# Kernel optimization log

Measured on AMD Instinct MI355X. Metric: run time of the kernel, lower is better.

## Reference

```python
import jax, jax.numpy as jnp
import numpy as np

L, H, A, E, V = 2, 512, 200, 512, 10000
SOS_ID = 0


def setup_inputs() -> dict:
    key = jax.random.key(0)
    ks = jax.random.split(key, 20)
    B, T, S = 64, 512, 128
    s = 0.02
    d = {}
    d["encoder_outputs"] = jax.random.normal(ks[0], (L, T, B, H), jnp.float32)
    d["encoder_final_states"] = jax.random.normal(ks[1], (L, B, H), jnp.float32)
    d["targets"] = jax.random.randint(ks[2], (B, S), 0, V)
    # Bahdanau attention params (per RNN layer)
    d["Qw"] = jax.random.normal(ks[3], (L, A, H), jnp.float32) * s
    d["Qb"] = jnp.zeros((L, A), jnp.float32)
    d["Kw"] = jax.random.normal(ks[4], (L, A, H), jnp.float32) * s
    d["Kb"] = jnp.zeros((L, A), jnp.float32)
    d["Vw"] = jax.random.normal(ks[5], (L, A), jnp.float32) * s
    d["Vb"] = jnp.zeros((L,), jnp.float32)
    # embedding table
    d["emb_table"] = jax.random.normal(ks[6], (V, E), jnp.float32) * s
    # 2-layer GRU (torch layout: W_ih (3H, in), W_hh (3H, H))
    d["Wih0"] = jax.random.normal(ks[7], (3 * H, E + H), jnp.float32) * s
    d["Whh0"] = jax.random.normal(ks[8], (3 * H, H), jnp.float32) * s
    d["bih0"] = jnp.zeros((3 * H,), jnp.float32)
    d["bhh0"] = jnp.zeros((3 * H,), jnp.float32)
    d["Wih1"] = jax.random.normal(ks[9], (3 * H, H), jnp.float32) * s
    d["Whh1"] = jax.random.normal(ks[10], (3 * H, H), jnp.float32) * s
    d["bih1"] = jnp.zeros((3 * H,), jnp.float32)
    d["bhh1"] = jnp.zeros((3 * H,), jnp.float32)
    # output projection (single Linear: decoder_projection=[])
    d["Pw"] = jax.random.normal(ks[11], (V, H), jnp.float32) * s
    d["Pb"] = jnp.zeros((V,), jnp.float32)
    return d


def _gru_cell(x, h, Wih, Whh, bih, bhh):
    gi = x @ Wih.T + bih
    gh = h @ Whh.T + bhh
    ir, iz, inn = jnp.split(gi, 3, axis=-1)
    hr, hz, hn = jnp.split(gh, 3, axis=-1)
    r = jax.nn.sigmoid(ir + hr)
    z = jax.nn.sigmoid(iz + hz)
    n = jnp.tanh(inn + r * hn)
    return (1.0 - z) * n + z * h


def reference(encoder_outputs, encoder_final_states, targets, Qw, Qb, Kw, Kb, Vw, Vb,
              emb_table, Wih0, Whh0, bih0, bhh0, Wih1, Whh1, bih1, bhh1, Pw, Pb):
    B, S = targets.shape
    # teacher forcing: input at step i is SOS for i=0 else targets[:, i-1]
    tok = jnp.concatenate([jnp.full((B, 1), SOS_ID, targets.dtype), targets[:, :-1]], axis=1)
    # keys don't change across steps -> precompute key projection: (L, T, B, A)
    k_proj = jnp.einsum('lah,ltbh->ltba', Kw, encoder_outputs) + Kb[:, None, None, :]

    def step(h, tok_t):
        # Bahdanau attention (softmax jointly over layers and time, per batch col)
        q = jnp.einsum('lah,lbh->lba', Qw, h) + Qb[:, None, :]          # (L,B,A)
        e = jnp.tanh(q[:, None] + k_proj)                                # (L,T,B,A)
        scores = jnp.einsum('la,ltba->ltb', Vw, e) + Vb[:, None, None]   # (L,T,B)
        w = jax.nn.softmax(scores.reshape(L * scores.shape[1], B), axis=0).reshape(scores.shape)
        context = jnp.einsum('ltb,ltbh->bh', w, encoder_outputs)         # (B,H)
        # embedding (+relu; dropout=0 / eval), concat with context
        x = jnp.concatenate([jax.nn.relu(emb_table[tok_t]), context], axis=-1)  # (B, E+H)
        h0 = _gru_cell(x, h[0], Wih0, Whh0, bih0, bhh0)
        h1 = _gru_cell(h0, h[1], Wih1, Whh1, bih1, bhh1)
        logits = h1 @ Pw.T + Pb                                           # (B,V)
        return jnp.stack([h0, h1]), logits

    _, logits = jax.lax.scan(step, encoder_final_states, tok.T)  # over S steps
    return jnp.transpose(logits, (1, 0, 2))  # (B, S, V)
```

## Files before the change

### kernel.cpp

```cpp
#include <hip/hip_runtime.h>


#define DEV __device__ __forceinline__

DEV float bf2f(unsigned short u) {
    unsigned int x = ((unsigned int)u) << 16;
    return __builtin_bit_cast(float, x);
}
DEV unsigned short f2bf(float f) {
    unsigned int x = __builtin_bit_cast(unsigned int, f);
    unsigned int r = (x + 0x7FFFu + ((x >> 16) & 1u)) >> 16;
    return (unsigned short)r;
}
DEV float fin(float v) {
    unsigned int b = __builtin_bit_cast(unsigned int, v);
    return ((b & 0x7F800000u) == 0x7F800000u) ? 1000.0f : v;
}
DEV float rcp_f(float x) { return __builtin_amdgcn_rcpf(x); }
DEV float sigm_f(float x) {
    x = fminf(fmaxf(x, -30.f), 30.f);
    float e = __expf(-x);
    return rcp_f(1.f + e);
}
DEV float tanh_f(float x) {
    x = fminf(fmaxf(x, -15.f), 15.f);
    float ex = __expf(2.f * x);
    return 1.f - 2.f * rcp_f(1.f + ex);
}

typedef __attribute__((ext_vector_type(8))) short short8;
typedef __attribute__((ext_vector_type(4))) float float4v;

__global__ __launch_bounds__(256) void detect_k(const unsigned short* __restrict__ raw,
                                                int* __restrict__ flag) {
    __shared__ int cnt;
    if (threadIdx.x == 0) cnt = 0;
    __syncthreads();
    long idx = 2L * ((long)threadIdx.x * 997 + 13);
    unsigned short u = raw[idx];
    unsigned int e = (u >> 7) & 0xFF;
    if (e >= 0x81) atomicAdd(&cnt, 1);
    __syncthreads();
    if (threadIdx.x == 0) *flag = (cnt >= 40) ? 1 : 0;
}

__global__ __launch_bounds__(256) void conv_k(const void* __restrict__ src,
                                              unsigned short* __restrict__ dst, long n,
                                              const int* __restrict__ flag) {
    int f = *flag;
    long i0 = (long)blockIdx.x * 256 + threadIdx.x;
    long st = (long)gridDim.x * 256;
    if (f) {
        const float* s = (const float*)src;
        for (long i = i0; i < n; i += st) dst[i] = f2bf(s[i]);
    } else {
        const unsigned short* s = (const unsigned short*)src;
        for (long i = i0; i < n; i += st) dst[i] = s[i];
    }
}

__global__ __launch_bounds__(256) void init_ht_k(const void* __restrict__ ef,
                                                 float* __restrict__ hT,
                                                 const int* __restrict__ flag) {
    int f = *flag;
    int i = blockIdx.x * 256 + threadIdx.x;
    int l = i >> 15, rem = i & 32767, b = rem >> 9, h = rem & 511;
    float v = f ? ((const float*)ef)[i] : bf2f(((const unsigned short*)ef)[i]);
    hT[(l * 512 + h) * 64 + b] = v;
}

__global__ __launch_bounds__(256) void mfma_gemm_k(
    const unsigned short* __restrict__ A, const void* __restrict__ BtV,
    const void* __restrict__ biasV, void* __restrict__ dstV, int Nlim, int mode,
    long Az, long Bz, long biasz, const int* __restrict__ flagp) {
    const int K = 512;
    int f = (mode == 1) ? *flagp : 0;
    int l = blockIdx.z;
    const unsigned short* Ab = A + (long)l * Az;
    const unsigned short* Bb = (const unsigned short*)BtV + (long)l * Bz;
    const float* Bf = (const float*)BtV + (long)l * Bz;
    int tid = threadIdx.x;
    int lane = tid & 63, wid = tid >> 6;
    int wy = wid >> 1, wx = wid & 1;
    int quad = lane >> 4, r16 = lane & 15;
    int m0 = blockIdx.x * 128 + wy * 64;
    int n0 = blockIdx.y * 128 + wx * 64;

    float4v acc[4][4];
    for (int i = 0; i < 4; ++i)
        for (int j = 0; j < 4; ++j) acc[i][j] = (float4v){0.f, 0.f, 0.f, 0.f};

    for (int kt = 0; kt < K / 32; ++kt) {
        int k0 = kt * 32 + quad * 8;
        short8 af[4], bfr[4];
#pragma unroll
        for (int mi = 0; mi < 4; ++mi) {
            int row = m0 + mi * 16 + r16;
            af[mi] = *(const short8*)(Ab + (long)row * K + k0);
        }
#pragma unroll
        for (int ni = 0; ni < 4; ++ni) {
            int col = n0 + ni * 16 + r16;
            if (col < Nlim) {
                if (f) {
                    short8 t;
#pragma unroll
                    for (int j = 0; j < 8; ++j)
                        t[j] = (short)f2bf(Bf[(long)col * K + k0 + j]);
                    bfr[ni] = t;
                } else {
                    bfr[ni] = *(const short8*)(Bb + (long)col * K + k0);
                }
            } else {
                bfr[ni] = (short8){0, 0, 0, 0, 0, 0, 0, 0};
            }
        }
#pragma unroll
        for (int mi = 0; mi < 4; ++mi)
#pragma unroll
            for (int ni = 0; ni < 4; ++ni)
                acc[mi][ni] = __builtin_amdgcn_mfma_f32_16x16x32_bf16(
                    af[mi], bfr[ni], acc[mi][ni], 0, 0, 0);
    }

    unsigned short* dstu = (unsigned short*)dstV;
    float* dstf = (float*)dstV;
    for (int mi = 0; mi < 4; ++mi)
        for (int ni = 0; ni < 4; ++ni) {
            int n = n0 + ni * 16 + r16;
            if (n >= Nlim) continue;
            float bv;
            if (mode == 0)
                bv = bf2f(((const unsigned short*)biasV)[l * biasz + n]);
            else
                bv = f ? ((const float*)biasV)[n] : bf2f(((const unsigned short*)biasV)[n]);
#pragma unroll
            for (int r = 0; r < 4; ++r) {
                int m = m0 + mi * 16 + quad * 4 + r;
                float v = fin(acc[mi][ni][r] + bv);
                if (mode == 0) {
                    int t = m >> 6, b = m & 63;
                    dstu[(((long)(l * 512 + t) * 200 + n) * 64 + b)] = f2bf(v);
                } else {
                    int s = m >> 6, b = m & 63;
                    long oi = ((long)b * 128 + s) * 10000 + n;
                    if (f) dstf[oi] = v;
                    else dstu[oi] = f2bf(v);
                }
            }
        }
}

__global__ __launch_bounds__(256) void q_k(const unsigned short* __restrict__ Qw,
                                           const unsigned short* __restrict__ Qb,
                                           const float* __restrict__ hT,
                                           float* __restrict__ q) {
    __shared__ float red[4][64];
    int blk = blockIdx.x;
    int l = blk / 200, a = blk % 200;
    int tid = threadIdx.x, w = tid >> 6, lane = tid & 63;
    const unsigned short* qr = Qw + (l * 200 + a) * 512;
    const float* hb = hT + l * 512 * 64;
    float acc = 0.f;
    int h0 = w * 128;
    for (int h = h0; h < h0 + 128; h += 8) {
        uint4 u = *(const uint4*)(qr + h);
        const unsigned short* us = (const unsigned short*)&u;
#pragma unroll
        for (int j = 0; j < 8; ++j) acc = fmaf(bf2f(us[j]), hb[(h + j) * 64 + lane], acc);
    }
    red[w][lane] = acc;
    __syncthreads();
    if (w == 0) {
        float v = red[0][lane] + red[1][lane] + red[2][lane] + red[3][lane] +
                  bf2f(Qb[l * 200 + a]);
        q[(l * 200 + a) * 64 + lane] = v;
    }
}

__global__ __launch_bounds__(256) void step1_k(
    const unsigned short* __restrict__ kp, const float* __restrict__ q,
    float* __restrict__ sc, const unsigned short* __restrict__ Vw,
    const unsigned short* __restrict__ Vb, const float* __restrict__ hT,
    const unsigned short* __restrict__ Whh0, const unsigned short* __restrict__ Whh1,
    const unsigned short* __restrict__ bhh0, const unsigned short* __restrict__ bhh1,
    float* __restrict__ gh, const unsigned short* __restrict__ emb,
    const int* __restrict__ tgt, float* __restrict__ xT, int s) {
    int blk = blockIdx.x, tid = threadIdx.x, w = tid >> 6, lane = tid & 63;
    if (blk < 256) {
        int l = blk >> 7, tc = blk & 127, t = tc * 4 + w;
        const unsigned short* kr = kp + (size_t)((l * 512 + t) * 200) * 64;
        const float* qb = q + (l * 200) * 64;
        float acc = 0.f;
#pragma unroll 4
        for (int a = 0; a < 200; ++a) {
            float x = bf2f(kr[a * 64 + lane]) + qb[a * 64 + lane];
            acc = fmaf(bf2f(Vw[l * 200 + a]), tanh_f(x), acc);
        }
        sc[(l * 512 + t) * 64 + lane] = acc + bf2f(Vb[l]);
    } else if (blk < 1024) {
        int widx = (blk - 256) * 4 + w;
        int layer = widx / 1536, j = widx % 1536;
        const unsigned short* Wr = (layer ? Whh1 : Whh0) + (size_t)j * 512;
        const float* hb = hT + layer * 512 * 64;
        float acc = 0.f;
        for (int h = 0; h < 512; h += 8) {
            uint4 u = *(const uint4*)(Wr + h);
            const unsigned short* us = (const unsigned short*)&u;
#pragma unroll
            for (int jj = 0; jj < 8; ++jj)
                acc = fmaf(bf2f(us[jj]), hb[(h + jj) * 64 + lane], acc);
        }
        acc += bf2f((layer ? bhh1 : bhh0)[j]);
        gh[(layer * 1536 + j) * 64 + lane] = acc;
    } else {
        int eb = blk - 1024;
        for (int it = 0; it < 16; ++it) {
            int i = eb * 4096 + it * 256 + tid;
            int b = i >> 9, k = i & 511;
            int tok = (s == 0) ? 0 : tgt[b * 128 + (s - 1)];
            tok = tok < 0 ? 0 : (tok > 9999 ? 9999 : tok);
            float v = bf2f(emb[(size_t)tok * 512 + k]);
            xT[k * 64 + b] = v > 0.f ? v : 0.f;
        }
    }
}

__global__ __launch_bounds__(256) void ctx_k(const float* __restrict__ sc,
                                             const unsigned short* __restrict__ enc,
                                             float* __restrict__ xT) {
    __shared__ float wbuf[1024];
    __shared__ float rbuf[256];
    int blk = blockIdx.x, tid = threadIdx.x;
    int b = blk >> 2, hq = blk & 3;

    float s0[4];
    float lm = -3.0e38f;
#pragma unroll
    for (int i = 0; i < 4; ++i) {
        float v = sc[(tid + i * 256) * 64 + b];
        v = fminf(fmaxf(v, -1.0e30f), 1.0e30f);
        s0[i] = v;
        lm = fmaxf(lm, v);
    }
    rbuf[tid] = lm;
    __syncthreads();
    for (int off = 128; off > 0; off >>= 1) {
        if (tid < off) rbuf[tid] = fmaxf(rbuf[tid], rbuf[tid + off]);
        __syncthreads();
    }
    float M = rbuf[0];
    __syncthreads();
    float ls = 0.f;
#pragma unroll
    for (int i = 0; i < 4; ++i) {
        float e = __expf(fmaxf(s0[i] - M, -80.f));
        wbuf[tid + i * 256] = e;
        ls += e;
    }
    rbuf[tid] = ls;
    __syncthreads();
    for (int off = 128; off > 0; off >>= 1) {
        if (tid < off) rbuf[tid] += rbuf[tid + off];
        __syncthreads();
    }
    float rinv = 1.0f / rbuf[0];

    int h = hq * 128 + (tid & 127), half = tid >> 7;
    float acc = 0.f;
#pragma unroll 8
    for (int lt = half * 512; lt < half * 512 + 512; ++lt)
        acc = fmaf(wbuf[lt], bf2f(enc[((size_t)lt * 64 + b) * 512 + h]), acc);
    __syncthreads();
    rbuf[tid] = acc;
    __syncthreads();
    if (tid < 128)
        xT[(512 + hq * 128 + tid) * 64 + b] = (rbuf[tid] + rbuf[tid + 128]) * rinv;
}

__global__ __launch_bounds__(256) void gru0_k(const float* __restrict__ xT,
                                              const unsigned short* __restrict__ Wih0,
                                              const unsigned short* __restrict__ bih0,
                                              const float* __restrict__ gh,
                                              float* __restrict__ hT) {
    __shared__ float red[4][6][64];
    int blk = blockIdx.x, tid = threadIdx.x, w = tid >> 6, lane = tid & 63;
    int jj0 = blk * 2;
    const unsigned short* r_[6];
    r_[0] = Wih0 + (size_t)(jj0) * 1024;
    r_[1] = Wih0 + (size_t)(jj0 + 1) * 1024;
    r_[2] = Wih0 + (size_t)(jj0 + 512) * 1024;
    r_[3] = Wih0 + (size_t)(jj0 + 513) * 1024;
    r_[4] = Wih0 + (size_t)(jj0 + 1024) * 1024;
    r_[5] = Wih0 + (size_t)(jj0 + 1025) * 1024;
    float acc[6] = {0.f, 0.f, 0.f, 0.f, 0.f, 0.f};
    int k0 = w * 256;
    for (int k = k0; k < k0 + 256; k += 8) {
        uint4 u[6];
#pragma unroll
        for (int i = 0; i < 6; ++i) u[i] = *(const uint4*)(r_[i] + k);
#pragma unroll
        for (int j = 0; j < 8; ++j) {
            float xv = xT[(k + j) * 64 + lane];
#pragma unroll
            for (int i = 0; i < 6; ++i)
                acc[i] = fmaf(bf2f(((const unsigned short*)&u[i])[j]), xv, acc[i]);
        }
    }
#pragma unroll
    for (int i = 0; i < 6; ++i) red[w][i][lane] = acc[i];
    __syncthreads();
    if (w == 0) {
#pragma unroll
        for (int d = 0; d < 2; ++d) {
            int j = jj0 + d;
            float gir = red[0][0 + d][lane] + red[1][0 + d][lane] + red[2][0 + d][lane] +
                        red[3][0 + d][lane] + bf2f(bih0[j]);
            float giz = red[0][2 + d][lane] + red[1][2 + d][lane] + red[2][2 + d][lane] +
                        red[3][2 + d][lane] + bf2f(bih0[512 + j]);
            float gin = red[0][4 + d][lane] + red[1][4 + d][lane] + red[2][4 + d][lane] +
                        red[3][4 + d][lane] + bf2f(bih0[1024 + j]);
            float r = sigm_f(gir + gh[j * 64 + lane]);
            float z = sigm_f(giz + gh[(512 + j) * 64 + lane]);
            float n = tanh_f(gin + r * gh[(1024 + j) * 64 + lane]);
            float hp = hT[j * 64 + lane];
            hT[j * 64 + lane] = (1.f - z) * n + z * hp;
        }
    }
}

__global__ __launch_bounds__(256) void gru1_k(float* __restrict__ hT,
                                              const unsigned short* __restrict__ Wih1,
                                              const unsigned short* __restrict__ bih1,
                                              const float* __restrict__ gh,
                                              unsigned short* __restrict__ h1a, int s) {
    __shared__ float red[4][6][64];
    int blk = blockIdx.x, tid = threadIdx.x, w = tid >> 6, lane = tid & 63;
    int jj0 = blk * 2;
    const float* x = hT;
    float* h1 = hT + 512 * 64;
    const float* gh1 = gh + 1536 * 64;
    const unsigned short* r_[6];
    r_[0] = Wih1 + (size_t)(jj0) * 512;
    r_[1] = Wih1 + (size_t)(jj0 + 1) * 512;
    r_[2] = Wih1 + (size_t)(jj0 + 512) * 512;
    r_[3] = Wih1 + (size_t)(jj0 + 513) * 512;
    r_[4] = Wih1 + (size_t)(jj0 + 1024) * 512;
    r_[5] = Wih1 + (size_t)(jj0 + 1025) * 512;
    float acc[6] = {0.f, 0.f, 0.f, 0.f, 0.f, 0.f};
    int k0 = w * 128;
    for (int k = k0; k < k0 + 128; k += 8) {
        uint4 u[6];
#pragma unroll
        for (int i = 0; i < 6; ++i) u[i] = *(const uint4*)(r_[i] + k);
#pragma unroll
        for (int j = 0; j < 8; ++j) {
            float xv = x[(k + j) * 64 + lane];
#pragma unroll
            for (int i = 0; i < 6; ++i)
                acc[i] = fmaf(bf2f(((const unsigned short*)&u[i])[j]), xv, acc[i]);
        }
    }
#pragma unroll
    for (int i = 0; i < 6; ++i) red[w][i][lane] = acc[i];
    __syncthreads();
    if (w == 0) {
#pragma unroll
        for (int d = 0; d < 2; ++d) {
            int j = jj0 + d;
            float gir = red[0][0 + d][lane] + red[1][0 + d][lane] + red[2][0 + d][lane] +
                        red[3][0 + d][lane] + bf2f(bih1[j]);
            float giz = red[0][2 + d][lane] + red[1][2 + d][lane] + red[2][2 + d][lane] +
                        red[3][2 + d][lane] + bf2f(bih1[512 + j]);
            float gin = red[0][4 + d][lane] + red[1][4 + d][lane] + red[2][4 + d][lane] +
                        red[3][4 + d][lane] + bf2f(bih1[1024 + j]);
            float r = sigm_f(gir + gh1[j * 64 + lane]);
            float z = sigm_f(giz + gh1[(512 + j) * 64 + lane]);
            float n = tanh_f(gin + r * gh1[(1024 + j) * 64 + lane]);
            float hp = h1[j * 64 + lane];
            float hn_ = fin((1.f - z) * n + z * hp);
            h1[j * 64 + lane] = hn_;
            h1a[((size_t)s * 64 + lane) * 512 + j] = f2bf(hn_);
        }
    }
}

extern "C" void kernel_launch(void* const* d_in, const int* in_sizes, int n_in,
                              void* d_out, int out_size, void* d_ws, size_t ws_size,
                              hipStream_t stream) {
    const void* enc = d_in[0];
    const void* efin = d_in[1];
    const int* tgt = (const int*)d_in[2];
    const void* Qw = d_in[3];
    const void* Qb = d_in[4];
    const void* Kw = d_in[5];
    const void* Kb = d_in[6];
    const void* Vw = d_in[7];
    const void* Vb = d_in[8];
    const void* emb = d_in[9];
    const void* Wih0 = d_in[10];
    const void* Whh0 = d_in[11];
    const void* bih0 = d_in[12];
    const void* bhh0 = d_in[13];
    const void* Wih1 = d_in[14];
    const void* Whh1 = d_in[15];
    const void* bih1 = d_in[16];
    const void* bhh1 = d_in[17];
    const void* Pw = d_in[18];
    const void* Pb = d_in[19];

    unsigned short* outa = (unsigned short*)d_out;
    unsigned short* kp = outa + 0L;
    unsigned short* enc_c = outa + 13107200L;
    unsigned short* emb_c = outa + 46661632L;
    unsigned short* Qw_c = outa + 51781632L;
    unsigned short* Kw_c = outa + 51986432L;
    unsigned short* Wih0_c = outa + 52191232L;
    unsigned short* Whh0_c = outa + 53764096L;
    unsigned short* Wih1_c = outa + 54550528L;
    unsigned short* Whh1_c = outa + 55336960L;
    unsigned short* sm = outa + 56123392L;
    unsigned short* Qb_c = sm + 0;
    unsigned short* Kb_c = sm + 408;
    unsigned short* Vw_c = sm + 816;
    unsigned short* Vb_c = sm + 1224;
    unsigned short* bih0_c = sm + 1232;
    unsigned short* bhh0_c = sm + 2768;
    unsigned short* bih1_c = sm + 4304;
    unsigned short* bhh1_c = sm + 5840;

    char* w = (char*)d_ws;
    int* flag = (int*)w;                       w += 256;
    float* hT = (float*)w;                     w += 262144;
    float* q = (float*)w;                      w += 102400;
    float* sc = (float*)w;                     w += 262144;
    float* xT = (float*)w;                     w += 262144;
    float* gh = (float*)w;                     w += 786432;
    unsigned short* h1a = (unsigned short*)w;  w += 8388608;

    detect_k<<<1, 256, 0, stream>>>((const unsigned short*)emb, flag);

    conv_k<<<2048, 256, 0, stream>>>(enc, enc_c, 33554432L, flag);
    conv_k<<<1024, 256, 0, stream>>>(emb, emb_c, 5120000L, flag);
    conv_k<<<256, 256, 0, stream>>>(Qw, Qw_c, 204800L, flag);
    conv_k<<<256, 256, 0, stream>>>(Kw, Kw_c, 204800L, flag);
    conv_k<<<512, 256, 0, stream>>>(Wih0, Wih0_c, 1572864L, flag);
    conv_k<<<256, 256, 0, stream>>>(Whh0, Whh0_c, 786432L, flag);
    conv_k<<<256, 256, 0, stream>>>(Wih1, Wih1_c, 786432L, flag);
    conv_k<<<256, 256, 0, stream>>>(Whh1, Whh1_c, 786432L, flag);
    conv_k<<<2, 256, 0, stream>>>(Qb, Qb_c, 400L, flag);
    conv_k<<<2, 256, 0, stream>>>(Kb, Kb_c, 400L, flag);
    conv_k<<<2, 256, 0, stream>>>(Vw, Vw_c, 400L, flag);
    conv_k<<<1, 256, 0, stream>>>(Vb, Vb_c, 2L, flag);
    conv_k<<<6, 256, 0, stream>>>(bih0, bih0_c, 1536L, flag);
    conv_k<<<6, 256, 0, stream>>>(bhh0, bhh0_c, 1536L, flag);
    conv_k<<<6, 256, 0, stream>>>(bih1, bih1_c, 1536L, flag);
    conv_k<<<6, 256, 0, stream>>>(bhh1, bhh1_c, 1536L, flag);

    init_ht_k<<<256, 256, 0, stream>>>(efin, hT, flag);

    mfma_gemm_k<<<dim3(256, 2, 2), 256, 0, stream>>>(
        enc_c, Kw_c, Kb_c, kp, 200, 0, (long)32768 * 512, (long)200 * 512, 200, flag);

    for (int s = 0; s < 128; ++s) {
        q_k<<<400, 256, 0, stream>>>(Qw_c, Qb_c, hT, q);
        step1_k<<<1032, 256, 0, stream>>>(kp, q, sc, Vw_c, Vb_c, hT, Whh0_c, Whh1_c,
                                          bhh0_c, bhh1_c, gh, emb_c, tgt, xT, s);
        ctx_k<<<256, 256, 0, stream>>>(sc, enc_c, xT);
        gru0_k<<<256, 256, 0, stream>>>(xT, Wih0_c, bih0_c, gh, hT);
        gru1_k<<<256, 256, 0, stream>>>(hT, Wih1_c, bih1_c, gh, h1a, s);
    }

    mfma_gemm_k<<<dim3(64, 79, 1), 256, 0, stream>>>(h1a, Pw, Pb, d_out, 10000, 1, 0,
                                                     0, 0, flag);
}
```

Before: 14.75 ms.

## Fuse per-step kernels into one persistent cooperative kernel with grid barriers

```diff
diff --git a/kernel.cpp b/kernel.cpp
--- a/kernel.cpp
+++ b/kernel.cpp
@@ -382,6 +382,268 @@
             h1[j * 64 + lane] = hn_;
             h1a[((size_t)s * 64 + lane) * 512 + j] = f2bf(hn_);
         }
+    }
+}
+
+DEV void gridbar(unsigned* bar, unsigned k) {
+    __syncthreads();
+    if (threadIdx.x == 0) {
+        __hip_atomic_fetch_add(bar + 32 + (blockIdx.x & 15) * 32, 1u,
+                               __ATOMIC_RELEASE, __HIP_MEMORY_SCOPE_AGENT);
+        if (blockIdx.x == 0) {
+            unsigned target = gridDim.x * k;
+            int guard = 0;
+            for (;;) {
+                unsigned sum = 0;
+#pragma unroll
+                for (int i = 0; i < 16; ++i)
+                    sum += __hip_atomic_load(bar + 32 + i * 32, __ATOMIC_RELAXED,
+                                             __HIP_MEMORY_SCOPE_AGENT);
+                if (sum >= target) break;
+                if (++guard > (1 << 15)) break;
+                __builtin_amdgcn_s_sleep(1);
+            }
+            __threadfence();
+            __hip_atomic_store(bar, k, __ATOMIC_RELEASE, __HIP_MEMORY_SCOPE_AGENT);
+        } else {
+            int guard = 0;
+            while (__hip_atomic_load(bar, __ATOMIC_RELAXED,
+                                     __HIP_MEMORY_SCOPE_AGENT) < k) {
+                if (++guard > (1 << 16)) break;
+                __builtin_amdgcn_s_sleep(2);
+            }
+            __threadfence();
+        }
+    }
+    __syncthreads();
+    __builtin_amdgcn_fence(__ATOMIC_ACQUIRE, "agent");
+}
+
+__global__ __launch_bounds__(256, 4) void step_loop_k(
+    const unsigned short* __restrict__ kp, const unsigned short* __restrict__ enc,
+    const unsigned short* __restrict__ emb, const int* __restrict__ tgt,
+    const unsigned short* __restrict__ Qw, const unsigned short* __restrict__ Qb,
+    const unsigned short* __restrict__ Vw, const unsigned short* __restrict__ Vb,
+    const unsigned short* __restrict__ Whh0, const unsigned short* __restrict__ Whh1,
+    const unsigned short* __restrict__ bhh0, const unsigned short* __restrict__ bhh1,
+    const unsigned short* __restrict__ Wih0, const unsigned short* __restrict__ bih0,
+    const unsigned short* __restrict__ Wih1, const unsigned short* __restrict__ bih1,
+    float* hT, float* q, float* sc, float* xT, float* gh,
+    unsigned short* h1a, unsigned* bar) {
+    int tid = threadIdx.x, w = tid >> 6, lane = tid & 63;
+    __shared__ float smem[1536];
+    unsigned bk = 0;
+
+    for (int s = 0; s < 128; ++s) {
+        for (unsigned u = blockIdx.x; u < 1176; u += gridDim.x) {
+            if (u < 400) {
+                int l = (int)u / 200, a = (int)u % 200;
+                const unsigned short* qr = Qw + (l * 200 + a) * 512;
+                const float* hb = hT + l * 512 * 64;
+                float acc = 0.f;
+                int h0 = w * 128;
+                for (int h = h0; h < h0 + 128; h += 8) {
+                    uint4 uu = *(const uint4*)(qr + h);
+                    const unsigned short* us = (const unsigned short*)&uu;
+#pragma unroll
+                    for (int j = 0; j < 8; ++j)
+                        acc = fmaf(bf2f(us[j]), hb[(h + j) * 64 + lane], acc);
+                }
+                float(*red)[64] = (float(*)[64])smem;
+                red[w][lane] = acc;
+                __syncthreads();
+                if (w == 0)
+                    q[(l * 200 + a) * 64 + lane] = red[0][lane] + red[1][lane] +
+                                                   red[2][lane] + red[3][lane] +
+                                                   bf2f(Qb[l * 200 + a]);
+            } else if (u < 1168) {
+                int widx = ((int)u - 400) * 4 + w;
+                int layer = widx / 1536, j = widx - layer * 1536;
+                const unsigned short* Wr = (layer ? Whh1 : Whh0) + (size_t)j * 512;
+                const float* hb = hT + layer * 512 * 64;
+                float acc = 0.f;
+                for (int h = 0; h < 512; h += 8) {
+                    uint4 uu = *(const uint4*)(Wr + h);
+                    const unsigned short* us = (const unsigned short*)&uu;
+#pragma unroll
+                    for (int jj = 0; jj < 8; ++jj)
+                        acc = fmaf(bf2f(us[jj]), hb[(h + jj) * 64 + lane], acc);
+                }
+                acc += bf2f((layer ? bhh1 : bhh0)[j]);
+                gh[(layer * 1536 + j) * 64 + lane] = acc;
+            } else {
+                int eb = (int)u - 1168;
+                for (int it = 0; it < 16; ++it) {
+                    int i = eb * 4096 + it * 256 + tid;
+                    int b = i >> 9, k = i & 511;
+                    int tok = (s == 0) ? 0 : tgt[b * 128 + (s - 1)];
+                    tok = tok < 0 ? 0 : (tok > 9999 ? 9999 : tok);
+                    float v = bf2f(emb[(size_t)tok * 512 + k]);
+                    xT[k * 64 + b] = v > 0.f ? v : 0.f;
+                }
+            }
+            __syncthreads();
+        }
+        gridbar(bar, ++bk);
+
+        for (unsigned u = blockIdx.x; u < 1024; u += gridDim.x) {
+            int l = (int)(u >> 9), t = (int)(u & 511);
+            const unsigned short* kr = kp + (size_t)((l * 512 + t) * 200) * 64;
+            const float* qb = q + (l * 200) * 64;
+            float acc = 0.f;
+            int a0 = w * 50;
+#pragma unroll 2
+            for (int a = a0; a < a0 + 50; ++a) {
+                float x = bf2f(kr[a * 64 + lane]) + qb[a * 64 + lane];
+                acc = fmaf(bf2f(Vw[l * 200 + a]), tanh_f(x), acc);
+            }
+            float(*red)[64] = (float(*)[64])smem;
+            red[w][lane] = acc;
+            __syncthreads();
+            if (w == 0)
+                sc[(l * 512 + t) * 64 + lane] = red[0][lane] + red[1][lane] +
+                                                red[2][lane] + red[3][lane] +
+                                                bf2f(Vb[l]);
+            __syncthreads();
+        }
+        gridbar(bar, ++bk);
+
+        for (unsigned u = blockIdx.x; u < 256; u += gridDim.x) {
+            int b = (int)(u >> 2), hq = (int)(u & 3);
+            float* wbuf = smem;
+            float* rbuf = smem + 1024;
+            float s0[4];
+            float lm = -3.0e38f;
+#pragma unroll
+            for (int i = 0; i < 4; ++i) {
+                float v = sc[(tid + i * 256) * 64 + b];
+                v = fminf(fmaxf(v, -1.0e30f), 1.0e30f);
+                s0[i] = v;
+                lm = fmaxf(lm, v);
+            }
+            rbuf[tid] = lm;
+            __syncthreads();
+            for (int off = 128; off > 0; off >>= 1) {
+                if (tid < off) rbuf[tid] = fmaxf(rbuf[tid], rbuf[tid + off]);
+                __syncthreads();
+            }
+            float M = rbuf[0];
+            __syncthreads();
+            float ls = 0.f;
+#pragma unroll
+            for (int i = 0; i < 4; ++i) {
+                float e = __expf(fmaxf(s0[i] - M, -80.f));
+                wbuf[tid + i * 256] = e;
+                ls += e;
+            }
+            rbuf[tid] = ls;
+            __syncthreads();
+            for (int off = 128; off > 0; off >>= 1) {
+                if (tid < off) rbuf[tid] += rbuf[tid + off];
+                __syncthreads();
+            }
+            float rinv = 1.0f / rbuf[0];
+
+            int h = hq * 128 + (tid & 127), half = tid >> 7;
+            float acc = 0.f;
+#pragma unroll 8
+            for (int lt = half * 512; lt < half * 512 + 512; ++lt)
+                acc = fmaf(wbuf[lt], bf2f(enc[((size_t)lt * 64 + b) * 512 + h]), acc);
+            __syncthreads();
+            rbuf[tid] = acc;
+            __syncthreads();
+            if (tid < 128)
+                xT[(512 + hq * 128 + tid) * 64 + b] = (rbuf[tid] + rbuf[tid + 128]) * rinv;
+            __syncthreads();
+        }
+        gridbar(bar, ++bk);
+
+        for (unsigned u = blockIdx.x; u < 512; u += gridDim.x) {
+            int j = (int)u;
+            const unsigned short* r0 = Wih0 + (size_t)j * 1024;
+            const unsigned short* r1 = Wih0 + (size_t)(512 + j) * 1024;
+            const unsigned short* r2 = Wih0 + (size_t)(1024 + j) * 1024;
+            float a0 = 0.f, a1 = 0.f, a2 = 0.f;
+            int k0 = w * 256;
+            for (int k = k0; k < k0 + 256; k += 8) {
+                uint4 u0 = *(const uint4*)(r0 + k);
+                uint4 u1 = *(const uint4*)(r1 + k);
+                uint4 u2 = *(const uint4*)(r2 + k);
+#pragma unroll
+                for (int jj = 0; jj < 8; ++jj) {
+                    float xv = xT[(k + jj) * 64 + lane];
+                    a0 = fmaf(bf2f(((const unsigned short*)&u0)[jj]), xv, a0);
+                    a1 = fmaf(bf2f(((const unsigned short*)&u1)[jj]), xv, a1);
+                    a2 = fmaf(bf2f(((const unsigned short*)&u2)[jj]), xv, a2);
+                }
+            }
+            float(*red)[3][64] = (float(*)[3][64])smem;
+            red[w][0][lane] = a0;
+            red[w][1][lane] = a1;
+            red[w][2][lane] = a2;
+            __syncthreads();
+            if (w == 0) {
+                float gir = red[0][0][lane] + red[1][0][lane] + red[2][0][lane] +
+                            red[3][0][lane] + bf2f(bih0[j]);
+                float giz = red[0][1][lane] + red[1][1][lane] + red[2][1][lane] +
+                            red[3][1][lane] + bf2f(bih0[512 + j]);
+                float gin = red[0][2][lane] + red[1][2][lane] + red[2][2][lane] +
+                            red[3][2][lane] + bf2f(bih0[1024 + j]);
+                float r = sigm_f(gir + gh[j * 64 + lane]);
+                float z = sigm_f(giz + gh[(512 + j) * 64 + lane]);
+                float n = tanh_f(gin + r * gh[(1024 + j) * 64 + lane]);
+                float hp = hT[j * 64 + lane];
+                hT[j * 64 + lane] = (1.f - z) * n + z * hp;
+            }
+            __syncthreads();
+        }
+        gridbar(bar, ++bk);
+
+        for (unsigned u = blockIdx.x; u < 512; u += gridDim.x) {
+            int j = (int)u;
+            const float* x = hT;
+            float* h1 = hT + 512 * 64;
+            const float* gh1 = gh + 1536 * 64;
+            const unsigned short* r0 = Wih1 + (size_t)j * 512;
+            const unsigned short* r1 = Wih1 + (size_t)(512 + j) * 512;
+            const unsigned short* r2 = Wih1 + (size_t)(1024 + j) * 512;
+            float a0 = 0.f, a1 = 0.f, a2 = 0.f;
+            int k0 = w * 128;
+            for (int k = k0; k < k0 + 128; k += 8) {
+                uint4 u0 = *(const uint4*)(r0 + k);
+                uint4 u1 = *(const uint4*)(r1 + k);
+                uint4 u2 = *(const uint4*)(r2 + k);
+#pragma unroll
+                for (int jj = 0; jj < 8; ++jj) {
+                    float xv = x[(k + jj) * 64 + lane];
+                    a0 = fmaf(bf2f(((const unsigned short*)&u0)[jj]), xv, a0);
+                    a1 = fmaf(bf2f(((const unsigned short*)&u1)[jj]), xv, a1);
+                    a2 = fmaf(bf2f(((const unsigned short*)&u2)[jj]), xv, a2);
+                }
+            }
+            float(*red)[3][64] = (float(*)[3][64])smem;
+            red[w][0][lane] = a0;
+            red[w][1][lane] = a1;
+            red[w][2][lane] = a2;
+            __syncthreads();
+            if (w == 0) {
+                float gir = red[0][0][lane] + red[1][0][lane] + red[2][0][lane] +
+                            red[3][0][lane] + bf2f(bih1[j]);
+                float giz = red[0][1][lane] + red[1][1][lane] + red[2][1][lane] +
+                            red[3][1][lane] + bf2f(bih1[512 + j]);
+                float gin = red[0][2][lane] + red[1][2][lane] + red[2][2][lane] +
+                            red[3][2][lane] + bf2f(bih1[1024 + j]);
+                float r = sigm_f(gir + gh1[j * 64 + lane]);
+                float z = sigm_f(giz + gh1[(512 + j) * 64 + lane]);
+                float n = tanh_f(gin + r * gh1[(1024 + j) * 64 + lane]);
+                float hp = h1[j * 64 + lane];
+                float hn_ = fin((1.f - z) * n + z * hp);
+                h1[j * 64 + lane] = hn_;
+                h1a[((size_t)s * 64 + lane) * 512 + j] = f2bf(hn_);
+            }
+            __syncthreads();
+        }
+        gridbar(bar, ++bk);
     }
 }
 
@@ -428,6 +690,7 @@
     unsigned short* bhh0_c = sm + 2768;
     unsigned short* bih1_c = sm + 4304;
     unsigned short* bhh1_c = sm + 5840;
+    unsigned* bar = (unsigned*)(outa + 57000000L);
 
     char* w = (char*)d_ws;
     int* flag = (int*)w;                       w += 256;
@@ -439,6 +702,7 @@
     unsigned short* h1a = (unsigned short*)w;  w += 8388608;
 
     detect_k<<<1, 256, 0, stream>>>((const unsigned short*)emb, flag);
+    hipMemsetAsync(bar, 0, (32 + 16 * 32) * sizeof(unsigned), stream);
 
     conv_k<<<2048, 256, 0, stream>>>(enc, enc_c, 33554432L, flag);
     conv_k<<<1024, 256, 0, stream>>>(emb, emb_c, 5120000L, flag);
@@ -462,13 +726,53 @@
     mfma_gemm_k<<<dim3(256, 2, 2), 256, 0, stream>>>(
         enc_c, Kw_c, Kb_c, kp, 200, 0, (long)32768 * 512, (long)200 * 512, 200, flag);
 
-    for (int s = 0; s < 128; ++s) {
-        q_k<<<400, 256, 0, stream>>>(Qw_c, Qb_c, hT, q);
-        step1_k<<<1032, 256, 0, stream>>>(kp, q, sc, Vw_c, Vb_c, hT, Whh0_c, Whh1_c,
-                                          bhh0_c, bhh1_c, gh, emb_c, tgt, xT, s);
-        ctx_k<<<256, 256, 0, stream>>>(sc, enc_c, xT);
-        gru0_k<<<256, 256, 0, stream>>>(xT, Wih0_c, bih0_c, gh, hT);
-        gru1_k<<<256, 256, 0, stream>>>(hT, Wih1_c, bih1_c, gh, h1a, s);
+    int maxb = 0;
+    if (hipOccupancyMaxActiveBlocksPerMultiprocessor(&maxb, (const void*)step_loop_k,
+                                                     256, 0) != hipSuccess ||
+        maxb <= 0)
+        maxb = 2;
+    long nbl = (long)maxb * 256;
+    int nb = (int)(nbl > 1024 ? 1024 : nbl);
+
+    const unsigned short* p_kp = kp;
+    const unsigned short* p_enc = enc_c;
+    const unsigned short* p_emb = emb_c;
+    const int* p_tgt = tgt;
+    const unsigned short* p_Qw = Qw_c;
+    const unsigned short* p_Qb = Qb_c;
+    const unsigned short* p_Vw = Vw_c;
+    const unsigned short* p_Vb = Vb_c;
+    const unsigned short* p_Whh0 = Whh0_c;
+    const unsigned short* p_Whh1 = Whh1_c;
+    const unsigned short* p_bhh0 = bhh0_c;
+    const unsigned short* p_bhh1 = bhh1_c;
+    const unsigned short* p_Wih0 = Wih0_c;
+    const unsigned short* p_bih0 = bih0_c;
+    const unsigned short* p_Wih1 = Wih1_c;
+    const unsigned short* p_bih1 = bih1_c;
+    float* p_hT = hT;
+    float* p_q = q;
+    float* p_sc = sc;
+    float* p_xT = xT;
+    float* p_gh = gh;
+    unsigned short* p_h1a = h1a;
+    unsigned* p_bar = bar;
+    void* cargs[] = {&p_kp,   &p_enc,  &p_emb,  &p_tgt,  &p_Qw,   &p_Qb,
+                     &p_Vw,   &p_Vb,   &p_Whh0, &p_Whh1, &p_bhh0, &p_bhh1,
+                     &p_Wih0, &p_bih0, &p_Wih1, &p_bih1, &p_hT,   &p_q,
+                     &p_sc,   &p_xT,   &p_gh,   &p_h1a,  &p_bar};
+    hipError_t ce = hipLaunchCooperativeKernel((const void*)step_loop_k, dim3(nb),
+                                               dim3(256), cargs, 0, stream);
+    if (ce != hipSuccess) {
+        for (int s = 0; s < 128; ++s) {
+            q_k<<<400, 256, 0, stream>>>(Qw_c, Qb_c, hT, q);
+            step1_k<<<1032, 256, 0, stream>>>(kp, q, sc, Vw_c, Vb_c, hT, Whh0_c,
+                                              Whh1_c, bhh0_c, bhh1_c, gh, emb_c, tgt,
+                                              xT, s);
+            ctx_k<<<256, 256, 0, stream>>>(sc, enc_c, xT);
+            gru0_k<<<256, 256, 0, stream>>>(xT, Wih0_c, bih0_c, gh, hT);
+            gru1_k<<<256, 256, 0, stream>>>(hT, Wih1_c, bih1_c, gh, h1a, s);
+        }
     }
 
     mfma_gemm_k<<<dim3(64, 79, 1), 256, 0, stream>>>(h1a, Pw, Pb, d_out, 10000, 1, 0,
```

After: 32.85 ms. 123% more time.
